# Optimization experiments

Measured on AMD Instinct MI355X. Metric: run time of the kernel, lower is better.

## Reference

```python
import jax, jax.numpy as jnp
import numpy as np

EPS = 1e-8

def hamilton(q1, q2):
    # q1, q2: (..., 4, D) with broadcasting; components along axis -2
    w1, x1, y1, z1 = (q1[..., i, :] for i in range(4))
    w2, x2, y2, z2 = (q2[..., i, :] for i in range(4))
    w = w1 * w2 - x1 * x2 - y1 * y2 - z1 * z2
    x = w1 * x2 + x1 * w2 + y1 * z2 - z1 * y2
    y = w1 * y2 - x1 * z2 + y1 * w2 + z1 * x2
    z = w1 * z2 + x1 * y2 - y1 * x2 + z1 * w2
    return jnp.stack([w, x, y, z], axis=-2)

def _normalize(q):
    # normalize over the 4-component axis (axis 0), as in the torch module
    return q / jnp.sqrt(jnp.sum(q * q, axis=0, keepdims=True) + EPS)

def setup_inputs() -> dict:
    key = jax.random.key(0)
    k1, k2, k3, k4 = jax.random.split(key, 4)
    B, T, d_model = 4, 4096, 1024
    quat_dim = d_model // 4
    x = jax.random.normal(k1, (B, T, d_model), dtype=jnp.float32)
    q_left = jax.random.normal(k2, (4, quat_dim), dtype=jnp.float32)
    q_right = jax.random.normal(k3, (4, quat_dim), dtype=jnp.float32)
    spectral_gate = jax.random.uniform(k4, (1, 1, 1, quat_dim), dtype=jnp.float32)
    return {"x": x, "q_left": q_left, "q_right": q_right, "spectral_gate": spectral_gate}

def reference(x, q_left, q_right, spectral_gate):
    B, T, d_model = x.shape
    quat_dim = d_model // 4
    x_quat = x.reshape(B, T, 4, quat_dim)
    # FFT over the time axis (torch dim=1), real spectral gate, real part of IFFT
    x_spectral = jnp.fft.fft(x_quat, axis=1)
    x_filtered = jnp.fft.ifft(x_spectral * spectral_gate, axis=1).real.astype(x.dtype)
    q_left_n = _normalize(q_left)
    q_right_n = _normalize(q_right)
    conj_sign = jnp.array([1.0, -1.0, -1.0, -1.0], dtype=x.dtype)[:, None]
    q_right_conj = q_right_n * conj_sign
    # vectorized over B and T at once (original loops over T)
    x_right = hamilton(x_filtered, q_right_conj)          # (B, T, 4, quat_dim)
    x_rotated = hamilton(q_left_n, x_right)               # broadcast q_left over (B, T)
    return x_rotated.reshape(B, T, d_model)
```

## Files before the change

kernel.cpp:

```cpp
#include <hip/hip_runtime.h>


constexpr int QD = 256;
constexpr int DM = 1024;
constexpr float EPS = 1e-8f;

__global__ __launch_bounds__(256) void ham_evo_kernel(
    const float* __restrict__ x,
    const float* __restrict__ ql,
    const float* __restrict__ qr,
    const float* __restrict__ gate,
    float* __restrict__ out,
    int total)
{
    const int tid0   = blockIdx.x * blockDim.x + threadIdx.x;
    const int stride = gridDim.x * blockDim.x;
    const int d4     = (tid0 & 63) * 4;

    float L[4][4], R[4][4], G[4];
    {
        float4 t;
        #pragma unroll
        for (int c = 0; c < 4; ++c) {
            t = *reinterpret_cast<const float4*>(ql + c * QD + d4);
            L[c][0] = t.x; L[c][1] = t.y; L[c][2] = t.z; L[c][3] = t.w;
            t = *reinterpret_cast<const float4*>(qr + c * QD + d4);
            R[c][0] = t.x; R[c][1] = t.y; R[c][2] = t.z; R[c][3] = t.w;
        }
        t = *reinterpret_cast<const float4*>(gate + d4);
        G[0] = t.x; G[1] = t.y; G[2] = t.z; G[3] = t.w;
    }

    float pw[4], px[4], py[4], pz[4];
    float rw[4], rx[4], ry[4], rz[4];
    #pragma unroll
    for (int j = 0; j < 4; ++j) {
        float sl = L[0][j]*L[0][j] + L[1][j]*L[1][j] + L[2][j]*L[2][j] + L[3][j]*L[3][j] + EPS;
        float il = rsqrtf(sl);
        pw[j] = L[0][j]*il; px[j] = L[1][j]*il; py[j] = L[2][j]*il; pz[j] = L[3][j]*il;
        float sr = R[0][j]*R[0][j] + R[1][j]*R[1][j] + R[2][j]*R[2][j] + R[3][j]*R[3][j] + EPS;
        float ir = rsqrtf(sr);
        rw[j] =  R[0][j]*ir;
        rx[j] = -R[1][j]*ir;
        ry[j] = -R[2][j]*ir;
        rz[j] = -R[3][j]*ir;
    }

    for (int i = tid0; i < total; i += stride) {
        const int bt = i >> 6;
        const float* xb = x   + (size_t)bt * DM + d4;
        float*       ob = out + (size_t)bt * DM + d4;

        float4 vw = *reinterpret_cast<const float4*>(xb + 0 * QD);
        float4 vx = *reinterpret_cast<const float4*>(xb + 1 * QD);
        float4 vy = *reinterpret_cast<const float4*>(xb + 2 * QD);
        float4 vz = *reinterpret_cast<const float4*>(xb + 3 * QD);

        const float fw[4] = {vw.x, vw.y, vw.z, vw.w};
        const float fx[4] = {vx.x, vx.y, vx.z, vx.w};
        const float fy[4] = {vy.x, vy.y, vy.z, vy.w};
        const float fz[4] = {vz.x, vz.y, vz.z, vz.w};
        float ow[4], ox[4], oy[4], oz[4];

        #pragma unroll
        for (int j = 0; j < 4; ++j) {
            const float aw = fw[j] * G[j];
            const float ax = fx[j] * G[j];
            const float ay = fy[j] * G[j];
            const float az = fz[j] * G[j];
            const float tw = aw*rw[j] - ax*rx[j] - ay*ry[j] - az*rz[j];
            const float tx = aw*rx[j] + ax*rw[j] + ay*rz[j] - az*ry[j];
            const float ty = aw*ry[j] - ax*rz[j] + ay*rw[j] + az*rx[j];
            const float tz = aw*rz[j] + ax*ry[j] - ay*rx[j] + az*rw[j];
            ow[j] = pw[j]*tw - px[j]*tx - py[j]*ty - pz[j]*tz;
            ox[j] = pw[j]*tx + px[j]*tw + py[j]*tz - pz[j]*ty;
            oy[j] = pw[j]*ty - px[j]*tz + py[j]*tw + pz[j]*tx;
            oz[j] = pw[j]*tz + px[j]*ty - py[j]*tx + pz[j]*tw;
        }

        *reinterpret_cast<float4*>(ob + 0 * QD) = make_float4(ow[0], ow[1], ow[2], ow[3]);
        *reinterpret_cast<float4*>(ob + 1 * QD) = make_float4(ox[0], ox[1], ox[2], ox[3]);
        *reinterpret_cast<float4*>(ob + 2 * QD) = make_float4(oy[0], oy[1], oy[2], oy[3]);
        *reinterpret_cast<float4*>(ob + 3 * QD) = make_float4(oz[0], oz[1], oz[2], oz[3]);
    }
}

extern "C" void kernel_launch(void* const* d_in, const int* in_sizes, int n_in,
                              void* d_out, int out_size, void* d_ws, size_t ws_size,
                              hipStream_t stream) {
    const float* x    = (const float*)d_in[0];
    const float* ql   = (const float*)d_in[1];
    const float* qr   = (const float*)d_in[2];
    const float* gate = (const float*)d_in[3];
    float* out = (float*)d_out;

    const int n_bt  = out_size / DM;
    const int total = n_bt * (QD / 4);

    const int block = 256;
    int grid = (total + block - 1) / block;
    if (grid > 2048) grid = 2048;

    ham_evo_kernel<<<grid, block, 0, stream>>>(x, ql, qr, gate, out, total);
}
```

Baseline: 116.2 us.

## Precompute quaternion params in a prologue kernel and use nontemporal float2 streaming

Adds a tiny prologue kernel that normalizes q_left and q_right and folds the spectral gate into the right quaternion, writing the results to workspace. The main kernel drops its grid-stride loop for one element pair per thread, loads the precomputed parameters, and streams x and out with 8-byte nontemporal loads and stores. This removes the per-thread normalization and the gate multiply and is meant to cut cache pollution. In exchange it adds a second kernel launch, uses narrower memory accesses than the previous float4 path, and launches a much larger grid.

```diff
diff --git a/kernel.cpp b/kernel.cpp
--- a/kernel.cpp
+++ b/kernel.cpp
@@ -5,84 +5,91 @@
 constexpr int DM = 1024;
 constexpr float EPS = 1e-8f;
 
-__global__ __launch_bounds__(256) void ham_evo_kernel(
+__global__ void ham_params_kernel(const float* __restrict__ ql,
+                                  const float* __restrict__ qr,
+                                  const float* __restrict__ gate,
+                                  float* __restrict__ ws) {
+    const int d = threadIdx.x;
+    const float l0 = ql[0*QD+d], l1 = ql[1*QD+d], l2 = ql[2*QD+d], l3 = ql[3*QD+d];
+    const float r0 = qr[0*QD+d], r1 = qr[1*QD+d], r2 = qr[2*QD+d], r3 = qr[3*QD+d];
+    const float g  = gate[d];
+    const float il = rsqrtf(l0*l0 + l1*l1 + l2*l2 + l3*l3 + EPS);
+    const float gr = g * rsqrtf(r0*r0 + r1*r1 + r2*r2 + r3*r3 + EPS);
+    ws[0*QD+d] = l0*il;  ws[1*QD+d] = l1*il;
+    ws[2*QD+d] = l2*il;  ws[3*QD+d] = l3*il;
+    ws[4*QD+d] =  r0*gr; ws[5*QD+d] = -r1*gr;
+    ws[6*QD+d] = -r2*gr; ws[7*QD+d] = -r3*gr;
+}
+
+__device__ __forceinline__ float2 ntload2(const float* p) {
+    union { unsigned long long u; float2 f; } c;
+    c.u = __builtin_nontemporal_load(reinterpret_cast<const unsigned long long*>(p));
+    return c.f;
+}
+__device__ __forceinline__ void ntstore2(float* p, float a, float b) {
+    union { unsigned long long u; float2 f; } c;
+    c.f = make_float2(a, b);
+    __builtin_nontemporal_store(c.u, reinterpret_cast<unsigned long long*>(p));
+}
+
+__device__ __forceinline__ void sandwich(
+    float aw, float ax, float ay, float az,
+    float pw, float px, float py, float pz,
+    float rw, float rx, float ry, float rz,
+    float& ow, float& ox, float& oy, float& oz)
+{
+    const float tw = aw*rw - ax*rx - ay*ry - az*rz;
+    const float tx = aw*rx + ax*rw + ay*rz - az*ry;
+    const float ty = aw*ry - ax*rz + ay*rw + az*rx;
+    const float tz = aw*rz + ax*ry - ay*rx + az*rw;
+    ow = pw*tw - px*tx - py*ty - pz*tz;
+    ox = pw*tx + px*tw + py*tz - pz*ty;
+    oy = pw*ty - px*tz + py*tw + pz*tx;
+    oz = pw*tz + px*ty - py*tx + pz*tw;
+}
+
+__global__ __launch_bounds__(256, 8) void ham_evo_kernel(
     const float* __restrict__ x,
-    const float* __restrict__ ql,
-    const float* __restrict__ qr,
-    const float* __restrict__ gate,
-    float* __restrict__ out,
-    int total)
+    const float* __restrict__ ws,
+    float* __restrict__ out)
 {
-    const int tid0   = blockIdx.x * blockDim.x + threadIdx.x;
-    const int stride = gridDim.x * blockDim.x;
-    const int d4     = (tid0 & 63) * 4;
+    const int i  = blockIdx.x * 256 + threadIdx.x;
+    const int bt = i >> 7;
+    const int c2 = (i & 127) * 2;
 
-    float L[4][4], R[4][4], G[4];
-    {
-        float4 t;
-        #pragma unroll
-        for (int c = 0; c < 4; ++c) {
-            t = *reinterpret_cast<const float4*>(ql + c * QD + d4);
-            L[c][0] = t.x; L[c][1] = t.y; L[c][2] = t.z; L[c][3] = t.w;
-            t = *reinterpret_cast<const float4*>(qr + c * QD + d4);
-            R[c][0] = t.x; R[c][1] = t.y; R[c][2] = t.z; R[c][3] = t.w;
-        }
-        t = *reinterpret_cast<const float4*>(gate + d4);
-        G[0] = t.x; G[1] = t.y; G[2] = t.z; G[3] = t.w;
-    }
+    const float* pb = ws + c2;
+    const float2 P0 = *reinterpret_cast<const float2*>(pb + 0*QD);
+    const float2 P1 = *reinterpret_cast<const float2*>(pb + 1*QD);
+    const float2 P2 = *reinterpret_cast<const float2*>(pb + 2*QD);
+    const float2 P3 = *reinterpret_cast<const float2*>(pb + 3*QD);
+    const float2 R0 = *reinterpret_cast<const float2*>(pb + 4*QD);
+    const float2 R1 = *reinterpret_cast<const float2*>(pb + 5*QD);
+    const float2 R2 = *reinterpret_cast<const float2*>(pb + 6*QD);
+    const float2 R3 = *reinterpret_cast<const float2*>(pb + 7*QD);
 
-    float pw[4], px[4], py[4], pz[4];
-    float rw[4], rx[4], ry[4], rz[4];
-    #pragma unroll
-    for (int j = 0; j < 4; ++j) {
-        float sl = L[0][j]*L[0][j] + L[1][j]*L[1][j] + L[2][j]*L[2][j] + L[3][j]*L[3][j] + EPS;
-        float il = rsqrtf(sl);
-        pw[j] = L[0][j]*il; px[j] = L[1][j]*il; py[j] = L[2][j]*il; pz[j] = L[3][j]*il;
-        float sr = R[0][j]*R[0][j] + R[1][j]*R[1][j] + R[2][j]*R[2][j] + R[3][j]*R[3][j] + EPS;
-        float ir = rsqrtf(sr);
-        rw[j] =  R[0][j]*ir;
-        rx[j] = -R[1][j]*ir;
-        ry[j] = -R[2][j]*ir;
-        rz[j] = -R[3][j]*ir;
-    }
+    const size_t base = (size_t)bt * DM + c2;
+    const float* xb = x + base;
+    float*       ob = out + base;
 
-    for (int i = tid0; i < total; i += stride) {
-        const int bt = i >> 6;
-        const float* xb = x   + (size_t)bt * DM + d4;
-        float*       ob = out + (size_t)bt * DM + d4;
+    const float2 xw = ntload2(xb + 0*QD);
+    const float2 xx = ntload2(xb + 1*QD);
+    const float2 xy = ntload2(xb + 2*QD);
+    const float2 xz = ntload2(xb + 3*QD);
 
-        float4 vw = *reinterpret_cast<const float4*>(xb + 0 * QD);
-        float4 vx = *reinterpret_cast<const float4*>(xb + 1 * QD);
-        float4 vy = *reinterpret_cast<const float4*>(xb + 2 * QD);
-        float4 vz = *reinterpret_cast<const float4*>(xb + 3 * QD);
+    float ow0, ox0, oy0, oz0, ow1, ox1, oy1, oz1;
+    sandwich(xw.x, xx.x, xy.x, xz.x,
+             P0.x, P1.x, P2.x, P3.x,
+             R0.x, R1.x, R2.x, R3.x,
+             ow0, ox0, oy0, oz0);
+    sandwich(xw.y, xx.y, xy.y, xz.y,
+             P0.y, P1.y, P2.y, P3.y,
+             R0.y, R1.y, R2.y, R3.y,
+             ow1, ox1, oy1, oz1);
 
-        const float fw[4] = {vw.x, vw.y, vw.z, vw.w};
-        const float fx[4] = {vx.x, vx.y, vx.z, vx.w};
-        const float fy[4] = {vy.x, vy.y, vy.z, vy.w};
-        const float fz[4] = {vz.x, vz.y, vz.z, vz.w};
-        float ow[4], ox[4], oy[4], oz[4];
-
-        #pragma unroll
-        for (int j = 0; j < 4; ++j) {
-            const float aw = fw[j] * G[j];
-            const float ax = fx[j] * G[j];
-            const float ay = fy[j] * G[j];
-            const float az = fz[j] * G[j];
-            const float tw = aw*rw[j] - ax*rx[j] - ay*ry[j] - az*rz[j];
-            const float tx = aw*rx[j] + ax*rw[j] + ay*rz[j] - az*ry[j];
-            const float ty = aw*ry[j] - ax*rz[j] + ay*rw[j] + az*rx[j];
-            const float tz = aw*rz[j] + ax*ry[j] - ay*rx[j] + az*rw[j];
-            ow[j] = pw[j]*tw - px[j]*tx - py[j]*ty - pz[j]*tz;
-            ox[j] = pw[j]*tx + px[j]*tw + py[j]*tz - pz[j]*ty;
-            oy[j] = pw[j]*ty - px[j]*tz + py[j]*tw + pz[j]*tx;
-            oz[j] = pw[j]*tz + px[j]*ty - py[j]*tx + pz[j]*tw;
-        }
-
-        *reinterpret_cast<float4*>(ob + 0 * QD) = make_float4(ow[0], ow[1], ow[2], ow[3]);
-        *reinterpret_cast<float4*>(ob + 1 * QD) = make_float4(ox[0], ox[1], ox[2], ox[3]);
-        *reinterpret_cast<float4*>(ob + 2 * QD) = make_float4(oy[0], oy[1], oy[2], oy[3]);
-        *reinterpret_cast<float4*>(ob + 3 * QD) = make_float4(oz[0], oz[1], oz[2], oz[3]);
-    }
+    ntstore2(ob + 0*QD, ow0, ow1);
+    ntstore2(ob + 1*QD, ox0, ox1);
+    ntstore2(ob + 2*QD, oy0, oy1);
+    ntstore2(ob + 3*QD, oz0, oz1);
 }
 
 extern "C" void kernel_launch(void* const* d_in, const int* in_sizes, int n_in,
@@ -93,13 +100,12 @@
     const float* qr   = (const float*)d_in[2];
     const float* gate = (const float*)d_in[3];
     float* out = (float*)d_out;
+    float* ws  = (float*)d_ws;
 
-    const int n_bt  = out_size / DM;
-    const int total = n_bt * (QD / 4);
+    ham_params_kernel<<<1, QD, 0, stream>>>(ql, qr, gate, ws);
 
-    const int block = 256;
-    int grid = (total + block - 1) / block;
-    if (grid > 2048) grid = 2048;
-
-    ham_evo_kernel<<<grid, block, 0, stream>>>(x, ql, qr, gate, out, total);
+    const int n_bt = out_size / DM;
+    const int total = n_bt * (QD / 2);
+    const int grid = total / 256;
+    ham_evo_kernel<<<grid, 256, 0, stream>>>(x, ws, out);
 }
```

Result: slower. 125.5 us (+7.9%).
